# Kernel tuning notes

Measured on AMD Instinct MI355X. Metric: run time of the kernel, lower is better.

Reference implementation:

```python
import jax, jax.numpy as jnp
import numpy as np

# --- FineRMoE routing constants (match init_kwargs) ---
TOP_K = 4
G_I, G_O = 2, 2
R_I, R_O = 4, 2
NUM_EXPERTS = 32  # must equal R_O*G_O*R_I*G_I


def _finermoe_router(scores):
    """scores: [T, E]. Returns (probs [T,top_k], selected [T,top_k])."""
    T, E = scores.shape
    S = E // (R_O * G_O)  # experts per concat-shard == R_I*G_I
    cs = scores.reshape(T, R_O * G_O, S)
    # top_k//G_O experts within each (R_O*G_O) shard
    _, add_idx = jax.lax.top_k(cs, TOP_K // G_O)
    add_mask = jnp.any(jax.nn.one_hot(add_idx, S, dtype=bool), axis=-2)  # [T, RO*GO, S]
    # keep the max-scoring R_O shard within each G_O group (argmax -> first max, like torch)
    shard_sum = cs.sum(-1).reshape(T, G_O, R_O)
    concat_mask = jax.nn.one_hot(jnp.argmax(shard_sum, axis=-1), R_O, dtype=bool)
    concat_mask = concat_mask.reshape(T, G_O * R_O)  # flat order matches RO*GO shard dim
    final_mask = (add_mask & concat_mask[:, :, None]).reshape(T, E)
    masked = jnp.where(final_mask, scores, -jnp.inf)
    probs, sel = jax.lax.top_k(masked, TOP_K)
    return probs, sel


def setup_inputs() -> dict:
    key = jax.random.key(0)
    ks = jax.random.split(key, 6)
    B, Sq, H, E, I = 1, 2048, 1024, NUM_EXPERTS, 256
    O = H // G_O  # expert output width
    return {
        "hidden_states": jax.random.normal(ks[0], (B, Sq, H), dtype=jnp.float32),
        "Wr": jax.random.normal(ks[1], (H, E), dtype=jnp.float32) * 0.02,
        "Wg": jax.random.normal(ks[2], (E, H, I), dtype=jnp.float32) * 0.02,
        "Wu": jax.random.normal(ks[3], (E, H, I), dtype=jnp.float32) * 0.02,
        "Wd": jax.random.normal(ks[4], (E, I, O), dtype=jnp.float32) * 0.02,
        "Wc": jax.random.normal(ks[5], (H, H), dtype=jnp.float32) * 0.02,
    }


def reference(hidden_states, Wr, Wg, Wu, Wd, Wc):
    B, Sq, H = hidden_states.shape
    T = B * Sq
    E = Wr.shape[1]
    x = hidden_states.reshape(T, H)
    router_logits = x @ Wr  # [T, E]
    probs, sel = _finermoe_router(router_logits)
    rw = jax.nn.softmax(probs.astype(jnp.float32), axis=1)
    rw = rw / rw.sum(-1, keepdims=True)  # norm_topk_prob
    rw = rw.astype(x.dtype)
    # dense combine weights [T, E] (zero for unselected experts)
    C = jnp.zeros((T, E), x.dtype).at[jnp.arange(T)[:, None], sel].add(rw)
    # all-expert MLP (stacked GEMMs); combine weights mask out unselected tokens
    h = jax.nn.silu(jnp.einsum('th,ehi->eti', x, Wg)) * jnp.einsum('th,ehi->eti', x, Wu)
    y = jnp.einsum('eti,eio->eto', h, Wd)  # [E, T, H//G_O]
    P = E // G_O  # experts per concat shard slice == R_O*G_I*R_I
    out = jnp.einsum('tgp,gpto->tgo', C.reshape(T, G_O, P),
                     y.reshape(G_O, P, T, H // G_O)).reshape(T, H)
    out = out @ Wc  # moe_concat_proj
    return out.reshape(B, Sq, H), router_logits
```

## Files before the change

kernel.cpp:

```cpp
#include <hip/hip_runtime.h>
#include <hip/hip_bf16.h>
#include <math.h>
#include <stdint.h>

typedef __hip_bfloat16 hbf16;

#define T_TOK 2048
#define H_DIM 1024
#define E_NUM 32
#define I_DIM 256
#define O_DIM 512
#define CAP   2048
#define TT    16
#define WT    16
#define XSTR2 520
#define HSTR  264

typedef __bf16 bf16x8 __attribute__((ext_vector_type(8)));
typedef float  f32x4  __attribute__((ext_vector_type(4)));

__device__ __forceinline__ float b2f(hbf16 v) { return __bfloat162float(v); }
__device__ __forceinline__ float bb2f(ushort u) { return __uint_as_float((uint32_t)u << 16); }

__device__ __forceinline__ ushort f2b(float f) {
    uint32_t u = __float_as_uint(f);
    return (ushort)((u + 0x7FFFu + ((u >> 16) & 1u)) >> 16);
}

template<int BF>
__device__ __forceinline__ float ld(const void* p, size_t i) {
    if (BF) return b2f(((const hbf16*)p)[i]);
    else    return ((const float*)p)[i];
}

__device__ __forceinline__ f32x4 mfma_bf16(bf16x8 a, bf16x8 b, f32x4 c) {
    return __builtin_amdgcn_mfma_f32_16x16x32_bf16(a, b, c, 0, 0, 0);
}

__device__ __forceinline__ void sched_fence() { __builtin_amdgcn_sched_barrier(0); }

__global__ __launch_bounds__(256) void detect_kernel(
    const uint32_t* __restrict__ xw, int* __restrict__ flag, int* __restrict__ counts)
{
    __shared__ int cnt;
    if (threadIdx.x == 0) cnt = 0;
    if (threadIdx.x < E_NUM) counts[threadIdx.x] = 0;
    __syncthreads();
    int c = 0;
    for (int i = threadIdx.x; i < 1024; i += 256) {
        int e = (xw[i] >> 7) & 0xFF;
        if (e >= 110 && e <= 140) c++;
    }
    atomicAdd(&cnt, c);
    __syncthreads();
    if (threadIdx.x == 0) *flag = (cnt > 512) ? 1 : 0;
}


__device__ void conv3_tile(const void* __restrict__ src, ushort* __restrict__ dst,
                           int bf, int K, int N, int b, float* __restrict__ sh)
{
    int tilesN = N >> 7, tilesK = K >> 5;
    int e  = b / (tilesK * tilesN);
    int r  = b % (tilesK * tilesN);
    int k0 = (r / tilesN) << 5;
    int n0 = (r % tilesN) << 7;
    size_t base = (size_t)e * K * N;
    int tid = threadIdx.x;
    {
        int row = tid >> 3, c0 = (tid & 7) * 16;
        if (!bf) {
            const float* sp = (const float*)src + base + (size_t)(k0 + row) * N + n0 + c0;
            #pragma unroll
            for (int i = 0; i < 4; ++i) {
                float4 v = *(const float4*)(sp + i * 4);
                sh[row * 132 + c0 + i*4 + 0] = v.x;
                sh[row * 132 + c0 + i*4 + 1] = v.y;
                sh[row * 132 + c0 + i*4 + 2] = v.z;
                sh[row * 132 + c0 + i*4 + 3] = v.w;
            }
        } else {
            const hbf16* sp = (const hbf16*)src + base + (size_t)(k0 + row) * N + n0 + c0;
            #pragma unroll
            for (int i = 0; i < 16; ++i) sh[row * 132 + c0 + i] = b2f(sp[i]);
        }
    }
    __syncthreads();
    {
        int nn = tid >> 1, kk = (tid & 1) * 16;
        union { ushort v[16]; uint4 u[2]; } R;
        #pragma unroll
        for (int i = 0; i < 16; ++i) R.v[i] = f2b(sh[(kk + i) * 132 + nn]);
        ushort* dp = dst + base + ((size_t)(k0 >> 5) * N + (n0 + nn)) * 32 + kk;
        *(uint4*)dp       = R.u[0];
        *(uint4*)(dp + 8) = R.u[1];
    }
    __syncthreads();
}

__global__ __launch_bounds__(256) void convert_all_kernel(
    const void* Wg, const void* Wu, const void* Wd, const void* Wc,
    ushort* Wg_t, ushort* Wu_t, ushort* Wd_t, ushort* Wc_t,
    const int* __restrict__ flag)
{
    __shared__ float sh[32 * 132];
    int bf = *flag;
    int b = blockIdx.x;
    if      (b < 2048) conv3_tile(Wg, Wg_t, bf, 1024,  256, b,        sh);
    else if (b < 4096) conv3_tile(Wu, Wu_t, bf, 1024,  256, b - 2048, sh);
    else if (b < 5120) conv3_tile(Wd, Wd_t, bf,  256,  512, b - 4096, sh);
    else               conv3_tile(Wc, Wc_t, bf, 1024, 1024, b - 5120, sh);
}

template<int BF>
__device__ void router3_body(const void* __restrict__ x, const void* __restrict__ Wr,
                             void* __restrict__ out_base,
                             int* __restrict__ counts, int* __restrict__ tok_list,
                             float* __restrict__ wt_list,
                             float* __restrict__ xs, float* __restrict__ wrs,
                             float* __restrict__ sl)
{
    int tid = threadIdx.x;
    int t0  = blockIdx.x * 8;
    int e   = tid & 31;
    int ta  = tid >> 5;

    float acc = 0.f;
    for (int k0 = 0; k0 < H_DIM; k0 += 128) {
        __syncthreads();
        {
            int tr = tid >> 5, c = (tid & 31) * 4;
            if (!BF) {
                *(float4*)&xs[tr * 128 + c] = *(const float4*)((const float*)x +
                                              (size_t)(t0 + tr) * H_DIM + k0 + c);
            } else {
                const hbf16* xp = (const hbf16*)x + (size_t)(t0 + tr) * H_DIM + k0 + c;
                xs[tr*128+c+0] = b2f(xp[0]); xs[tr*128+c+1] = b2f(xp[1]);
                xs[tr*128+c+2] = b2f(xp[2]); xs[tr*128+c+3] = b2f(xp[3]);
            }
        }
        for (int i = tid; i < 1024; i += 256) {
            if (!BF) {
                ((float4*)wrs)[i] = *((const float4*)((const float*)Wr + (size_t)k0 * 32) + i);
            } else {
                const hbf16* wp = (const hbf16*)Wr + (size_t)k0 * 32 + i * 4;
                wrs[i*4+0] = b2f(wp[0]); wrs[i*4+1] = b2f(wp[1]);
                wrs[i*4+2] = b2f(wp[2]); wrs[i*4+3] = b2f(wp[3]);
            }
        }
        __syncthreads();
        #pragma unroll 8
        for (int k = 0; k < 128; k += 4) {
            float4 xv = *(const float4*)&xs[ta * 128 + k];
            float w0 = wrs[(k+0)*32 + e];
            float w1 = wrs[(k+1)*32 + e];
            float w2 = wrs[(k+2)*32 + e];
            float w3 = wrs[(k+3)*32 + e];
            acc = fmaf(xv.w, w3, fmaf(xv.z, w2, fmaf(xv.y, w1, fmaf(xv.x, w0, acc))));
        }
    }
    sl[ta * 32 + e] = acc;
    size_t li = (size_t)T_TOK * H_DIM + (size_t)(t0 + ta) * E_NUM + e;
    if (BF) ((hbf16*)out_base)[li] = __float2bfloat16(acc);
    else    ((float*)out_base)[li] = acc;
    __syncthreads();

    if (tid < 8) {
        int t = t0 + tid;
        float s[E_NUM];
        #pragma unroll
        for (int i = 0; i < E_NUM; ++i) s[i] = sl[tid * 32 + i];

        int   selE[4];
        float selL[4];
        int ns = 0;
        for (int g = 0; g < 2; ++g) {
            float sum0 = 0.f, sum1 = 0.f;
            #pragma unroll
            for (int j = 0; j < 8; ++j) {
                sum0 += s[(2*g)   * 8 + j];
                sum1 += s[(2*g+1) * 8 + j];
            }
            int bestSh = (sum1 > sum0) ? (2*g+1) : (2*g);
            int base = bestSh * 8;
            int i1 = 0;
            for (int j = 1; j < 8; ++j) if (s[base+j] > s[base+i1]) i1 = j;
            int i2 = -1;
            for (int j = 0; j < 8; ++j) {
                if (j == i1) continue;
                if (i2 < 0 || s[base+j] > s[base+i2]) i2 = j;
            }
            selE[ns] = base + i1; selL[ns] = s[base+i1]; ++ns;
            selE[ns] = base + i2; selL[ns] = s[base+i2]; ++ns;
        }
        float m = fmaxf(fmaxf(selL[0], selL[1]), fmaxf(selL[2], selL[3]));
        float w[4];
        float sum = 0.f;
        for (int j = 0; j < 4; ++j) { w[j] = expf(selL[j] - m); sum += w[j]; }
        float inv = 1.f / sum;
        for (int j = 0; j < 4; ++j) {
            int ee = selE[j];
            int pos = atomicAdd(&counts[ee], 1);
            if (pos >= 0 && pos < CAP) {
                tok_list[ee * CAP + pos] = t | (j << 11);
                wt_list[ee * CAP + pos]  = w[j] * inv;
            }
        }
    }
}

__global__ __launch_bounds__(256) void router3_kernel(
    const void* x, const void* Wr, void* out_base, const int* flag,
    int* counts, int* tok_list, float* wt_list)
{
    __shared__ float xs[8 * 128];
    __shared__ float wrs[128 * 32];
    __shared__ float sl[8 * 32];
    if (*flag) router3_body<1>(x, Wr, out_base, counts, tok_list, wt_list, xs, wrs, sl);
    else       router3_body<0>(x, Wr, out_base, counts, tok_list, wt_list, xs, wrs, sl);
}

template<int BF>
__device__ void expert3_body(const void* __restrict__ x,
    const ushort* __restrict__ Wg_t, const ushort* __restrict__ Wu_t,
    const ushort* __restrict__ Wd_t,
    const int* __restrict__ counts, const int* __restrict__ tok_list,
    const float* __restrict__ wt_list, ushort* __restrict__ ybuf,
    ushort* __restrict__ xA, ushort* __restrict__ hsm,
    int* __restrict__ tokid, float* __restrict__ twt, int* __restrict__ tslot)
{
    int e = blockIdx.x;
    int n = counts[e]; n = n < 0 ? 0 : (n > CAP ? CAP : n);
    int t0 = blockIdx.y * 32;
    if (t0 >= n) return;
    int tid  = threadIdx.x;
    int lane = tid & 63, wv = tid >> 6;
    int q = lane >> 4, l15 = lane & 15;

    if (tid < 32) {
        int it = t0 + tid;
        int id; float ww;
        if (it < n) { id = tok_list[e*CAP + it]; ww = wt_list[e*CAP + it]; }
        else        { id = tok_list[e*CAP + t0]; ww = 0.f; }
        tokid[tid] = id & 2047;
        tslot[tid] = (id >> 11) & 3;
        twt[tid]   = ww;
    }
    __syncthreads();

    const ushort* Bg0 = Wg_t + (size_t)e * (H_DIM * I_DIM) + (wv*32 + l15) * 32 + q*8;
    const ushort* Bu0 = Wu_t + (size_t)e * (H_DIM * I_DIM) + (wv*32 + l15) * 32 + q*8;

    f32x4 Cg[2][2], Cu[2][2];
    #pragma unroll
    for (int m = 0; m < 2; ++m)
        #pragma unroll
        for (int j = 0; j < 2; ++j) { Cg[m][j] = (f32x4)0.f; Cu[m][j] = (f32x4)0.f; }

    bf16x8 bg[2][4][2], bu[2][4][2];
    #pragma unroll
    for (int ig = 0; ig < 4; ++ig)
        #pragma unroll
        for (int j = 0; j < 2; ++j) {
            bg[0][ig][j] = *(const bf16x8*)(Bg0 + (size_t)ig*8192 + j*512);
            bu[0][ig][j] = *(const bf16x8*)(Bu0 + (size_t)ig*8192 + j*512);
        }
    sched_fence();

    #pragma unroll
    for (int hk = 0; hk < 2; ++hk) {
        if (hk) __syncthreads();

        {
            int row = tid >> 4;
            int kb  = (tid & 15) * 8;
            size_t srow = (size_t)tokid[row] * H_DIM + hk * 512;
            #pragma unroll
            for (int c = 0; c < 4; ++c) {
                int k = kb + c * 128;
                union { ushort v[8]; uint4 u; } U;
                if (BF) {
                    U.u = *(const uint4*)((const ushort*)x + srow + k);
                } else {
                    const float* xp = (const float*)x + srow + k;
                    float4 a = *(const float4*)xp;
                    float4 b = *(const float4*)(xp + 4);
                    U.v[0]=f2b(a.x); U.v[1]=f2b(a.y); U.v[2]=f2b(a.z); U.v[3]=f2b(a.w);
                    U.v[4]=f2b(b.x); U.v[5]=f2b(b.y); U.v[6]=f2b(b.z); U.v[7]=f2b(b.w);
                }
                *(uint4*)&xA[row * XSTR2 + k] = U.u;
            }
        }
        __syncthreads();

        #pragma unroll
        for (int g2 = 0; g2 < 4; ++g2) {
            int grp = hk * 4 + g2;
            int cb  = grp & 1;
            if (grp < 7) {
                #pragma unroll
                for (int ig = 0; ig < 4; ++ig)
                    #pragma unroll
                    for (int j = 0; j < 2; ++j) {
                        int idx = (grp + 1) * 4 + ig;
                        bg[cb^1][ig][j] = *(const bf16x8*)(Bg0 + (size_t)idx*8192 + j*512);
                        bu[cb^1][ig][j] = *(const bf16x8*)(Bu0 + (size_t)idx*8192 + j*512);
                    }
            }
            sched_fence();
            #pragma unroll
            for (int ig = 0; ig < 4; ++ig) {
                int kl = (g2 * 4 + ig) * 32;
                bf16x8 A0 = *(const bf16x8*)&xA[(l15)      * XSTR2 + kl + q*8];
                bf16x8 A1 = *(const bf16x8*)&xA[(16 + l15) * XSTR2 + kl + q*8];
                #pragma unroll
                for (int j = 0; j < 2; ++j) {
                    Cg[0][j] = mfma_bf16(A0, bg[cb][ig][j], Cg[0][j]);
                    Cg[1][j] = mfma_bf16(A1, bg[cb][ig][j], Cg[1][j]);
                    Cu[0][j] = mfma_bf16(A0, bu[cb][ig][j], Cu[0][j]);
                    Cu[1][j] = mfma_bf16(A1, bu[cb][ig][j], Cu[1][j]);
                }
            }
        }
    }

    const ushort* Bd0 = Wd_t + (size_t)e * (I_DIM * O_DIM) + (wv*64 + l15) * 32 + q*8;
    bf16x8 bd[2][4][4];
    #pragma unroll
    for (int g2 = 0; g2 < 2; ++g2)
        #pragma unroll
        for (int kc2 = 0; kc2 < 4; ++kc2)
            #pragma unroll
            for (int j = 0; j < 4; ++j)
                bd[g2][kc2][j] = *(const bf16x8*)(Bd0 + (size_t)(g2*4 + kc2)*16384 + j*512);
    sched_fence();

    #pragma unroll
    for (int m = 0; m < 2; ++m)
        #pragma unroll
        for (int j = 0; j < 2; ++j)
            #pragma unroll
            for (int r = 0; r < 4; ++r) {
                float g = Cg[m][j][r], u = Cu[m][j][r];
                float h = (g / (1.f + expf(-g))) * u;
                hsm[(m*16 + q*4 + r) * HSTR + wv*32 + j*16 + l15] = f2b(h);
            }
    __syncthreads();

    f32x4 Cd[2][4];
    #pragma unroll
    for (int m = 0; m < 2; ++m)
        #pragma unroll
        for (int j = 0; j < 4; ++j) Cd[m][j] = (f32x4)0.f;

    #pragma unroll
    for (int g2 = 0; g2 < 2; ++g2)
        #pragma unroll
        for (int kc2 = 0; kc2 < 4; ++kc2) {
            int kc = g2 * 4 + kc2;
            bf16x8 A0 = *(const bf16x8*)&hsm[(l15)      * HSTR + kc*32 + q*8];
            bf16x8 A1 = *(const bf16x8*)&hsm[(16 + l15) * HSTR + kc*32 + q*8];
            #pragma unroll
            for (int j = 0; j < 4; ++j) {
                Cd[0][j] = mfma_bf16(A0, bd[g2][kc2][j], Cd[0][j]);
                Cd[1][j] = mfma_bf16(A1, bd[g2][kc2][j], Cd[1][j]);
            }
        }

    #pragma unroll
    for (int m = 0; m < 2; ++m)
        #pragma unroll
        for (int r = 0; r < 4; ++r) {
            int row = m*16 + q*4 + r;
            if (t0 + row < n) {
                float ww = twt[row];
                size_t base = ((size_t)tokid[row] * 4 + tslot[row]) * O_DIM;
                #pragma unroll
                for (int j = 0; j < 4; ++j)
                    ybuf[base + wv*64 + j*16 + l15] = f2b(ww * Cd[m][j][r]);
            }
        }
}

__global__ __launch_bounds__(512, 2) void expert3_kernel(
    const void* x, const ushort* Wg_t, const ushort* Wu_t, const ushort* Wd_t,
    const int* flag, const int* counts, const int* tok_list, const float* wt_list,
    ushort* ybuf)
{
    __shared__ ushort xA[32 * XSTR2];
    __shared__ ushort hsm[32 * HSTR];
    __shared__ int    tokid[32];
    __shared__ float  twt[32];
    __shared__ int    tslot[32];
    if (*flag) expert3_body<1>(x, Wg_t, Wu_t, Wd_t, counts, tok_list, wt_list,
                               ybuf, xA, hsm, tokid, twt, tslot);
    else       expert3_body<0>(x, Wg_t, Wu_t, Wd_t, counts, tok_list, wt_list,
                               ybuf, xA, hsm, tokid, twt, tslot);
}

template<int BF>
__device__ void wc3_body(const ushort* __restrict__ ybuf, const ushort* __restrict__ Wc_t,
                         void* __restrict__ out_base, ushort* __restrict__ zA)
{
    int m0  = blockIdx.x * 32;
    int n0  = blockIdx.y * 256;
    int tid = threadIdx.x;
    int lane = tid & 63, wv = tid >> 6;
    int q = lane >> 4, l15 = lane & 15;

    const ushort* Bc0 = Wc_t + (size_t)(n0 + wv*32 + l15) * 32 + q*8;
    f32x4 C[2][2];
    #pragma unroll
    for (int m = 0; m < 2; ++m)
        #pragma unroll
        for (int j = 0; j < 2; ++j) C[m][j] = (f32x4)0.f;

    bf16x8 bc[2][4][2];
    #pragma unroll
    for (int ig = 0; ig < 4; ++ig)
        #pragma unroll
        for (int j = 0; j < 2; ++j)
            bc[0][ig][j] = *(const bf16x8*)(Bc0 + (size_t)ig*32768 + j*512);
    sched_fence();

    #pragma unroll
    for (int hk = 0; hk < 2; ++hk) {
        if (hk) __syncthreads();

        {
            int row = tid >> 4;
            int kb  = (tid & 15) * 8;
            int t = m0 + row;
            int s0 = hk ? 2 : 0;
            #pragma unroll
            for (int c = 0; c < 4; ++c) {
                int hl = kb + c * 128;
                const ushort* p0 = ybuf + ((size_t)t * 4 + s0) * O_DIM + hl;
                union { ushort v[8]; uint4 u; } A, B, R;
                A.u = *(const uint4*)p0;
                B.u = *(const uint4*)(p0 + O_DIM);
                #pragma unroll
                for (int i = 0; i < 8; ++i) R.v[i] = f2b(bb2f(A.v[i]) + bb2f(B.v[i]));
                *(uint4*)&zA[row * XSTR2 + hl] = R.u;
            }
        }
        __syncthreads();

        #pragma unroll
        for (int g2 = 0; g2 < 4; ++g2) {
            int grp = hk * 4 + g2;
            int cb  = grp & 1;
            if (grp < 7) {
                #pragma unroll
                for (int ig = 0; ig < 4; ++ig)
                    #pragma unroll
                    for (int j = 0; j < 2; ++j) {
                        int idx = (grp + 1) * 4 + ig;
                        bc[cb^1][ig][j] = *(const bf16x8*)(Bc0 + (size_t)idx*32768 + j*512);
                    }
            }
            sched_fence();
            #pragma unroll
            for (int ig = 0; ig < 4; ++ig) {
                int kl = (g2 * 4 + ig) * 32;
                bf16x8 A0 = *(const bf16x8*)&zA[(l15)      * XSTR2 + kl + q*8];
                bf16x8 A1 = *(const bf16x8*)&zA[(16 + l15) * XSTR2 + kl + q*8];
                #pragma unroll
                for (int j = 0; j < 2; ++j) {
                    C[0][j] = mfma_bf16(A0, bc[cb][ig][j], C[0][j]);
                    C[1][j] = mfma_bf16(A1, bc[cb][ig][j], C[1][j]);
                }
            }
        }
    }

    #pragma unroll
    for (int m = 0; m < 2; ++m)
        #pragma unroll
        for (int j = 0; j < 2; ++j)
            #pragma unroll
            for (int r = 0; r < 4; ++r) {
                int row = m0 + m*16 + q*4 + r;
                int col = n0 + wv*32 + j*16 + l15;
                size_t o = (size_t)row * H_DIM + col;
                if (BF) ((hbf16*)out_base)[o] = __float2bfloat16(C[m][j][r]);
                else    ((float*)out_base)[o] = C[m][j][r];
            }
}

__global__ __launch_bounds__(512, 2) void wc3_kernel(
    const ushort* ybuf, const ushort* Wc_t, void* out_base, const int* flag)
{
    __shared__ ushort zA[32 * XSTR2];
    if (*flag) wc3_body<1>(ybuf, Wc_t, out_base, zA);
    else       wc3_body<0>(ybuf, Wc_t, out_base, zA);
}


__global__ __launch_bounds__(256) void zero_kernel(
    float* __restrict__ z_fp32, float* __restrict__ z_bf16,
    const int* __restrict__ flag, int* __restrict__ counts)
{
    float* base = (*flag) ? z_bf16 : z_fp32;
    size_t i = (size_t)blockIdx.x * 256 + threadIdx.x;
    ((float4*)base)[i] = make_float4(0.f, 0.f, 0.f, 0.f);
    if (blockIdx.x == 0 && threadIdx.x < E_NUM) counts[threadIdx.x] = 0;
}

template<int BF>
__device__ void router_body(const void* __restrict__ x, const void* __restrict__ Wr,
                            void* __restrict__ out_base,
                            int* __restrict__ counts, int* __restrict__ tok_list,
                            float* __restrict__ wt_list, float* __restrict__ sl)
{
    int t    = blockIdx.x;
    int lane = threadIdx.x;
    int e    = lane & 31;
    int half = lane >> 5;

    float acc = 0.f;
    size_t xoff = (size_t)t * H_DIM;
    int h0 = half * (H_DIM / 2);
    for (int h = h0; h < h0 + H_DIM / 2; ++h)
        acc = fmaf(ld<BF>(x, xoff + h), ld<BF>(Wr, (size_t)h * E_NUM + e), acc);
    acc += __shfl_down(acc, 32);

    if (lane < 32) {
        sl[e] = acc;
        size_t li = (size_t)T_TOK * H_DIM + (size_t)t * E_NUM + e;
        if (BF) ((hbf16*)out_base)[li] = __float2bfloat16(acc);
        else    ((float*)out_base)[li] = acc;
    }
    __syncthreads();

    if (lane == 0) {
        float s[E_NUM];
        #pragma unroll
        for (int i = 0; i < E_NUM; ++i) s[i] = sl[i];
        int   selE[4];
        float selL[4];
        int ns = 0;
        for (int g = 0; g < 2; ++g) {
            float sum0 = 0.f, sum1 = 0.f;
            #pragma unroll
            for (int j = 0; j < 8; ++j) {
                sum0 += s[(2*g)   * 8 + j];
                sum1 += s[(2*g+1) * 8 + j];
            }
            int bestSh = (sum1 > sum0) ? (2*g+1) : (2*g);
            int base = bestSh * 8;
            int i1 = 0;
            for (int j = 1; j < 8; ++j) if (s[base+j] > s[base+i1]) i1 = j;
            int i2 = -1;
            for (int j = 0; j < 8; ++j) {
                if (j == i1) continue;
                if (i2 < 0 || s[base+j] > s[base+i2]) i2 = j;
            }
            selE[ns] = base + i1; selL[ns] = s[base+i1]; ++ns;
            selE[ns] = base + i2; selL[ns] = s[base+i2]; ++ns;
        }
        float m = fmaxf(fmaxf(selL[0], selL[1]), fmaxf(selL[2], selL[3]));
        float w[4];
        float sum = 0.f;
        for (int j = 0; j < 4; ++j) { w[j] = expf(selL[j] - m); sum += w[j]; }
        float inv = 1.f / sum;
        for (int j = 0; j < 4; ++j) {
            int ee = selE[j];
            int pos = atomicAdd(&counts[ee], 1);
            if (pos >= 0 && pos < CAP) {
                tok_list[ee * CAP + pos] = t;
                wt_list[ee * CAP + pos]  = w[j] * inv;
            }
        }
    }
}

__global__ __launch_bounds__(64) void router_kernel(
    const void* x, const void* Wr, void* out_base, const int* flag,
    int* counts, int* tok_list, float* wt_list)
{
    __shared__ float sl[E_NUM];
    if (*flag) router_body<1>(x, Wr, out_base, counts, tok_list, wt_list, sl);
    else       router_body<0>(x, Wr, out_base, counts, tok_list, wt_list, sl);
}

template<int BF>
__device__ void expert_body(const void* __restrict__ x,
                            const void* __restrict__ Wg, const void* __restrict__ Wu,
                            const void* __restrict__ Wd,
                            const int* __restrict__ counts, const int* __restrict__ tok_list,
                            const float* __restrict__ wt_list,
                            float* __restrict__ z, float* __restrict__ xsbuf)
{
    int e = blockIdx.x;
    int n = counts[e];
    n = n < 0 ? 0 : (n > CAP ? CAP : n);
    int t0 = blockIdx.y * TT;
    if (t0 >= n) return;
    int tid = threadIdx.x;

    float (*xs)[H_DIM] = reinterpret_cast<float(*)[H_DIM]>(xsbuf);
    float (*hs)[I_DIM] = reinterpret_cast<float(*)[I_DIM]>(xsbuf);

    const int*   tl = tok_list + e * CAP;
    const float* wl = wt_list  + e * CAP;

    for (int idx = tid; idx < TT * H_DIM; idx += 256) {
        int tt = idx >> 10;
        int h  = idx & (H_DIM - 1);
        int it = t0 + tt;
        int tkn = (it < n) ? tl[it] : tl[t0];
        tkn = (tkn < 0) ? 0 : (tkn >= T_TOK ? T_TOK - 1 : tkn);
        xs[tt][h] = ld<BF>(x, (size_t)tkn * H_DIM + h);
    }
    __syncthreads();

    size_t wbase = (size_t)e * H_DIM * I_DIM + tid;
    float ag[TT], au[TT];
    #pragma unroll
    for (int tt = 0; tt < TT; ++tt) { ag[tt] = 0.f; au[tt] = 0.f; }

    for (int k = 0; k < H_DIM; k += 4) {
        float g0 = ld<BF>(Wg, wbase + (size_t)(k+0) * I_DIM);
        float g1 = ld<BF>(Wg, wbase + (size_t)(k+1) * I_DIM);
        float g2 = ld<BF>(Wg, wbase + (size_t)(k+2) * I_DIM);
        float g3 = ld<BF>(Wg, wbase + (size_t)(k+3) * I_DIM);
        float u0 = ld<BF>(Wu, wbase + (size_t)(k+0) * I_DIM);
        float u1 = ld<BF>(Wu, wbase + (size_t)(k+1) * I_DIM);
        float u2 = ld<BF>(Wu, wbase + (size_t)(k+2) * I_DIM);
        float u3 = ld<BF>(Wu, wbase + (size_t)(k+3) * I_DIM);
        #pragma unroll
        for (int tt = 0; tt < TT; ++tt) {
            float4 xv = *(const float4*)&xs[tt][k];
            ag[tt] = fmaf(xv.w, g3, fmaf(xv.z, g2, fmaf(xv.y, g1, fmaf(xv.x, g0, ag[tt]))));
            au[tt] = fmaf(xv.w, u3, fmaf(xv.z, u2, fmaf(xv.y, u1, fmaf(xv.x, u0, au[tt]))));
        }
    }
    float hval[TT];
    #pragma unroll
    for (int tt = 0; tt < TT; ++tt) {
        float g = ag[tt];
        hval[tt] = (g / (1.f + expf(-g))) * au[tt];
    }
    __syncthreads();
    #pragma unroll
    for (int tt = 0; tt < TT; ++tt) hs[tt][tid] = hval[tt];
    __syncthreads();

    size_t dbase = (size_t)e * I_DIM * O_DIM;
    float y0[TT], y1[TT];
    #pragma unroll
    for (int tt = 0; tt < TT; ++tt) { y0[tt] = 0.f; y1[tt] = 0.f; }

    for (int k = 0; k < I_DIM; k += 4) {
        float d00 = ld<BF>(Wd, dbase + (size_t)(k+0) * O_DIM + tid);
        float d01 = ld<BF>(Wd, dbase + (size_t)(k+1) * O_DIM + tid);
        float d02 = ld<BF>(Wd, dbase + (size_t)(k+2) * O_DIM + tid);
        float d03 = ld<BF>(Wd, dbase + (size_t)(k+3) * O_DIM + tid);
        float d10 = ld<BF>(Wd, dbase + (size_t)(k+0) * O_DIM + tid + 256);
        float d11 = ld<BF>(Wd, dbase + (size_t)(k+1) * O_DIM + tid + 256);
        float d12 = ld<BF>(Wd, dbase + (size_t)(k+2) * O_DIM + tid + 256);
        float d13 = ld<BF>(Wd, dbase + (size_t)(k+3) * O_DIM + tid + 256);
        #pragma unroll
        for (int tt = 0; tt < TT; ++tt) {
            float4 hv = *(const float4*)&hs[tt][k];
            y0[tt] = fmaf(hv.w, d03, fmaf(hv.z, d02, fmaf(hv.y, d01, fmaf(hv.x, d00, y0[tt]))));
            y1[tt] = fmaf(hv.w, d13, fmaf(hv.z, d12, fmaf(hv.y, d11, fmaf(hv.x, d10, y1[tt]))));
        }
    }

    int gsel = e >> 4;
    size_t colbase = (size_t)gsel * O_DIM;
    #pragma unroll
    for (int tt = 0; tt < TT; ++tt) {
        int it = t0 + tt;
        if (it < n) {
            float w  = wl[it];
            int tkn = tl[it];
            tkn = (tkn < 0) ? 0 : (tkn >= T_TOK ? T_TOK - 1 : tkn);
            atomicAdd(&z[(size_t)tkn * H_DIM + colbase + tid],       w * y0[tt]);
            atomicAdd(&z[(size_t)tkn * H_DIM + colbase + tid + 256], w * y1[tt]);
        }
    }
}

__global__ __launch_bounds__(256) void expert_kernel(
    const void* x, const void* Wg, const void* Wu, const void* Wd,
    const int* flag, const int* counts, const int* tok_list, const float* wt_list,
    float* z_fp32, float* z_bf16)
{
    __shared__ __align__(16) float xsbuf[TT * H_DIM];
    if (*flag) expert_body<1>(x, Wg, Wu, Wd, counts, tok_list, wt_list, z_bf16, xsbuf);
    else       expert_body<0>(x, Wg, Wu, Wd, counts, tok_list, wt_list, z_fp32, xsbuf);
}

template<int BF>
__device__ void wc_body(const float* __restrict__ z, const void* __restrict__ Wc,
                        void* __restrict__ out_base, float* __restrict__ psbuf)
{
    int t0  = blockIdx.x * WT;
    int tid = threadIdx.x;
    float (*ps)[H_DIM] = reinterpret_cast<float(*)[H_DIM]>(psbuf);

    for (int idx = tid; idx < WT * H_DIM; idx += 256) {
        int tt = idx >> 10;
        int h  = idx & (H_DIM - 1);
        ps[tt][h] = z[(size_t)(t0 + tt) * H_DIM + h];
    }
    __syncthreads();

    float acc[WT][4];
    #pragma unroll
    for (int tt = 0; tt < WT; ++tt)
        #pragma unroll
        for (int qq = 0; qq < 4; ++qq) acc[tt][qq] = 0.f;

    for (int k = 0; k < H_DIM; k += 2) {
        float c00 = ld<BF>(Wc, (size_t)(k+0) * H_DIM + tid);
        float c01 = ld<BF>(Wc, (size_t)(k+0) * H_DIM + tid + 256);
        float c02 = ld<BF>(Wc, (size_t)(k+0) * H_DIM + tid + 512);
        float c03 = ld<BF>(Wc, (size_t)(k+0) * H_DIM + tid + 768);
        float c10 = ld<BF>(Wc, (size_t)(k+1) * H_DIM + tid);
        float c11 = ld<BF>(Wc, (size_t)(k+1) * H_DIM + tid + 256);
        float c12 = ld<BF>(Wc, (size_t)(k+1) * H_DIM + tid + 512);
        float c13 = ld<BF>(Wc, (size_t)(k+1) * H_DIM + tid + 768);
        #pragma unroll
        for (int tt = 0; tt < WT; ++tt) {
            float2 pv = *(const float2*)&ps[tt][k];
            acc[tt][0] = fmaf(pv.y, c10, fmaf(pv.x, c00, acc[tt][0]));
            acc[tt][1] = fmaf(pv.y, c11, fmaf(pv.x, c01, acc[tt][1]));
            acc[tt][2] = fmaf(pv.y, c12, fmaf(pv.x, c02, acc[tt][2]));
            acc[tt][3] = fmaf(pv.y, c13, fmaf(pv.x, c03, acc[tt][3]));
        }
    }

    #pragma unroll
    for (int tt = 0; tt < WT; ++tt) {
        #pragma unroll
        for (int qq = 0; qq < 4; ++qq) {
            size_t o = (size_t)(t0 + tt) * H_DIM + tid + 256 * qq;
            if (BF) ((hbf16*)out_base)[o] = __float2bfloat16(acc[tt][qq]);
            else    ((float*)out_base)[o] = acc[tt][qq];
        }
    }
}

__global__ __launch_bounds__(256) void wc_kernel(
    const float* z_fp32, const float* z_bf16, const void* Wc,
    void* out_base, const int* flag)
{
    __shared__ __align__(16) float psbuf[WT * H_DIM];
    if (*flag) wc_body<1>(z_bf16, Wc, out_base, psbuf);
    else       wc_body<0>(z_fp32, Wc, out_base, psbuf);
}

extern "C" void kernel_launch(void* const* d_in, const int* in_sizes, int n_in,
                              void* d_out, int out_size, void* d_ws, size_t ws_size,
                              hipStream_t stream)
{
    (void)in_sizes; (void)n_in; (void)out_size;

    const void* x  = d_in[0];
    const void* Wr = d_in[1];
    const void* Wg = d_in[2];
    const void* Wu = d_in[3];
    const void* Wd = d_in[4];
    const void* Wc = d_in[5];

    char* ws = (char*)d_ws;
    int*   counts   = (int*)(ws + 0);
    int*   flag     = (int*)(ws + 128);
    int*   tok_list = (int*)(ws + 4096);
    float* wt_list  = (float*)(ws + 4096 + (size_t)E_NUM * CAP * 4);

    detect_kernel<<<1, 256, 0, stream>>>((const uint32_t*)x, flag, counts);

    if (ws_size >= ((size_t)58 << 20)) {
        ushort* ybuf = (ushort*)(ws + ((size_t)1  << 20));
        ushort* Wg_t = (ushort*)(ws + ((size_t)16 << 20));
        ushort* Wu_t = (ushort*)(ws + ((size_t)32 << 20));
        ushort* Wd_t = (ushort*)(ws + ((size_t)48 << 20));
        ushort* Wc_t = (ushort*)(ws + ((size_t)56 << 20));

        convert_all_kernel<<<5376, 256, 0, stream>>>(Wg, Wu, Wd, Wc,
                                                     Wg_t, Wu_t, Wd_t, Wc_t, flag);
        router3_kernel<<<T_TOK / 8, 256, 0, stream>>>(x, Wr, d_out, flag,
                                                      counts, tok_list, wt_list);
        expert3_kernel<<<dim3(E_NUM, T_TOK / 32), 512, 0, stream>>>(
            x, Wg_t, Wu_t, Wd_t, flag, counts, tok_list, wt_list, ybuf);
        wc3_kernel<<<dim3(T_TOK / 32, 4), 512, 0, stream>>>(ybuf, Wc_t, d_out, flag);
    } else {
        float* z_bf16 = (float*)(ws + (1u << 20));
        float* z_fp32 = (float*)d_out;
        zero_kernel<<<T_TOK, 256, 0, stream>>>(z_fp32, z_bf16, flag, counts);
        router_kernel<<<T_TOK, 64, 0, stream>>>(x, Wr, d_out, flag, counts, tok_list, wt_list);
        expert_kernel<<<dim3(E_NUM, T_TOK / TT), 256, 0, stream>>>(
            x, Wg, Wu, Wd, flag, counts, tok_list, wt_list, z_fp32, z_bf16);
        wc_kernel<<<T_TOK / WT, 256, 0, stream>>>(z_fp32, z_bf16, Wc, d_out, flag);
    }
}
```

Baseline: 254.0 us.

## Split router GEMV over K across warps with two tokens per block

The router kernel now handles 2 tokens per block instead of 8, so there are 1024 blocks. Each block's 8 warp-groups each take a 128-wide K slice, and the partial sums are reduced through shared memory. Wr is read directly from global memory per thread instead of being staged in LDS, which removes the K-loop syncs. The intent is more parallelism and a shorter serial dependency chain per block, at the cost of more total Wr reads and an extra reduction step.

```diff
diff --git a/kernel.cpp b/kernel.cpp
--- a/kernel.cpp
+++ b/kernel.cpp
@@ -117,59 +117,61 @@
                              void* __restrict__ out_base,
                              int* __restrict__ counts, int* __restrict__ tok_list,
                              float* __restrict__ wt_list,
-                             float* __restrict__ xs, float* __restrict__ wrs,
-                             float* __restrict__ sl)
-{
-    int tid = threadIdx.x;
-    int t0  = blockIdx.x * 8;
-    int e   = tid & 31;
-    int ta  = tid >> 5;
-
-    float acc = 0.f;
-    for (int k0 = 0; k0 < H_DIM; k0 += 128) {
-        __syncthreads();
-        {
-            int tr = tid >> 5, c = (tid & 31) * 4;
-            if (!BF) {
-                *(float4*)&xs[tr * 128 + c] = *(const float4*)((const float*)x +
-                                              (size_t)(t0 + tr) * H_DIM + k0 + c);
-            } else {
-                const hbf16* xp = (const hbf16*)x + (size_t)(t0 + tr) * H_DIM + k0 + c;
-                xs[tr*128+c+0] = b2f(xp[0]); xs[tr*128+c+1] = b2f(xp[1]);
-                xs[tr*128+c+2] = b2f(xp[2]); xs[tr*128+c+3] = b2f(xp[3]);
-            }
-        }
-        for (int i = tid; i < 1024; i += 256) {
-            if (!BF) {
-                ((float4*)wrs)[i] = *((const float4*)((const float*)Wr + (size_t)k0 * 32) + i);
-            } else {
-                const hbf16* wp = (const hbf16*)Wr + (size_t)k0 * 32 + i * 4;
-                wrs[i*4+0] = b2f(wp[0]); wrs[i*4+1] = b2f(wp[1]);
-                wrs[i*4+2] = b2f(wp[2]); wrs[i*4+3] = b2f(wp[3]);
-            }
-        }
-        __syncthreads();
-        #pragma unroll 8
-        for (int k = 0; k < 128; k += 4) {
-            float4 xv = *(const float4*)&xs[ta * 128 + k];
-            float w0 = wrs[(k+0)*32 + e];
-            float w1 = wrs[(k+1)*32 + e];
-            float w2 = wrs[(k+2)*32 + e];
-            float w3 = wrs[(k+3)*32 + e];
-            acc = fmaf(xv.w, w3, fmaf(xv.z, w2, fmaf(xv.y, w1, fmaf(xv.x, w0, acc))));
-        }
-    }
-    sl[ta * 32 + e] = acc;
-    size_t li = (size_t)T_TOK * H_DIM + (size_t)(t0 + ta) * E_NUM + e;
-    if (BF) ((hbf16*)out_base)[li] = __float2bfloat16(acc);
-    else    ((float*)out_base)[li] = acc;
-    __syncthreads();
-
-    if (tid < 8) {
+                             float* __restrict__ xs, float* __restrict__ sl,
+                             float* __restrict__ sf)
+{
+    int tid  = threadIdx.x;
+    int t0   = blockIdx.x * 2;
+    int e    = tid & 31;
+    int half = tid >> 5;
+
+    {
+        int t = tid >> 7;
+        int c = (tid & 127) * 8;
+        if (!BF) {
+            const float* xp = (const float*)x + (size_t)(t0 + t) * H_DIM + c;
+            *(float4*)&xs[t*1024 + c]     = *(const float4*)xp;
+            *(float4*)&xs[t*1024 + c + 4] = *(const float4*)(xp + 4);
+        } else {
+            const hbf16* xp = (const hbf16*)x + (size_t)(t0 + t) * H_DIM + c;
+            #pragma unroll
+            for (int j = 0; j < 8; ++j) xs[t*1024 + c + j] = b2f(xp[j]);
+        }
+    }
+    __syncthreads();
+
+    float a0 = 0.f, a1 = 0.f;
+    int kbase = half * 128;
+    const float* xr0 = &xs[kbase];
+    const float* xr1 = &xs[1024 + kbase];
+    #pragma unroll 8
+    for (int k = 0; k < 128; ++k) {
+        float w = ld<BF>(Wr, (size_t)(kbase + k) * E_NUM + e);
+        a0 = fmaf(xr0[k], w, a0);
+        a1 = fmaf(xr1[k], w, a1);
+    }
+    sl[(0*8 + half)*32 + e] = a0;
+    sl[(1*8 + half)*32 + e] = a1;
+    __syncthreads();
+
+    if (tid < 64) {
+        int t  = tid >> 5;
+        int ee = tid & 31;
+        float s = 0.f;
+        #pragma unroll
+        for (int h = 0; h < 8; ++h) s += sl[(t*8 + h)*32 + ee];
+        sf[t*32 + ee] = s;
+        size_t li = (size_t)T_TOK * H_DIM + (size_t)(t0 + t) * E_NUM + ee;
+        if (BF) ((hbf16*)out_base)[li] = __float2bfloat16(s);
+        else    ((float*)out_base)[li] = s;
+    }
+    __syncthreads();
+
+    if (tid < 2) {
         int t = t0 + tid;
         float s[E_NUM];
         #pragma unroll
-        for (int i = 0; i < E_NUM; ++i) s[i] = sl[tid * 32 + i];
+        for (int i = 0; i < E_NUM; ++i) s[i] = sf[tid * 32 + i];
 
         int   selE[4];
         float selL[4];
@@ -213,11 +215,11 @@
     const void* x, const void* Wr, void* out_base, const int* flag,
     int* counts, int* tok_list, float* wt_list)
 {
-    __shared__ float xs[8 * 128];
-    __shared__ float wrs[128 * 32];
-    __shared__ float sl[8 * 32];
-    if (*flag) router3_body<1>(x, Wr, out_base, counts, tok_list, wt_list, xs, wrs, sl);
-    else       router3_body<0>(x, Wr, out_base, counts, tok_list, wt_list, xs, wrs, sl);
+    __shared__ __align__(16) float xs[2 * 1024];
+    __shared__ float sl[2 * 8 * 32];
+    __shared__ float sf[2 * 32];
+    if (*flag) router3_body<1>(x, Wr, out_base, counts, tok_list, wt_list, xs, sl, sf);
+    else       router3_body<0>(x, Wr, out_base, counts, tok_list, wt_list, xs, sl, sf);
 }
 
 template<int BF>
@@ -784,7 +786,7 @@
 
         convert_all_kernel<<<5376, 256, 0, stream>>>(Wg, Wu, Wd, Wc,
                                                      Wg_t, Wu_t, Wd_t, Wc_t, flag);
-        router3_kernel<<<T_TOK / 8, 256, 0, stream>>>(x, Wr, d_out, flag,
+        router3_kernel<<<T_TOK / 2, 256, 0, stream>>>(x, Wr, d_out, flag,
                                                       counts, tok_list, wt_list);
         expert3_kernel<<<dim3(E_NUM, T_TOK / 32), 512, 0, stream>>>(
             x, Wg_t, Wu_t, Wd_t, flag, counts, tok_list, wt_list, ybuf);
```

Result: no change. 252.9 us (-0.4%).
